# Performance work log

Hardware: AMD Instinct MI355X
Metric: run time of the kernel (lower is better)

Reference implementation:

```python
import jax, jax.numpy as jnp
import numpy as np

R = 6                 # max displacement / padding
D = 2 * R + 1         # window side; D*D = 169 displacements


def setup_inputs() -> dict:
    key = jax.random.key(0)
    k1, k2, k3 = jax.random.split(key, 3)
    b, cf, h, w = 2, 32, 256, 256
    feats_t = jax.random.normal(k1, (b, cf, h, w), jnp.float32)
    feats_r = jax.random.normal(k2, (b, cf, h, w), jnp.float32)
    img_r = jax.random.uniform(k3, (b, 1, h, w), jnp.float32)
    return {"feats_t": feats_t, "feats_r": feats_r, "img_r": img_r}


def _forward(feats_t, feats_r, img_r):
    b, cf, h, w = feats_t.shape
    ci = img_r.shape[1]
    x2p = jnp.pad(feats_r, ((0, 0), (0, 0), (R, R), (R, R)))
    imgp = jnp.pad(img_r, ((0, 0), (0, 0), (R, R), (R, R)))
    # displacement offsets in the same order as the torch double loop (_y outer, _x inner)
    offs = jnp.stack(
        jnp.meshgrid(jnp.arange(D), jnp.arange(D), indexing="ij"), axis=-1
    ).reshape(-1, 2)

    def step(carry, off):
        dy, dx = off[0], off[1]
        win = jax.lax.dynamic_slice(x2p, (0, 0, dy, dx), (b, cf, h, w))
        c = jnp.sum(feats_t * win, axis=1)  # [b, h, w] correlation for this displacement
        iw = jax.lax.dynamic_slice(imgp, (0, 0, dy, dx), (b, ci, h, w))
        return carry, (c, iw)

    _, (corr, imgs) = jax.lax.scan(step, 0, offs)  # corr: [D*D, b, h, w]; imgs: [D*D, b, ci, h, w]
    attn = jax.nn.softmax(corr, axis=0)  # softmax over displacements (torch dim=1 channel axis)
    # weighted sum of shifted reference images -> warped target image
    return jnp.einsum("dbhw,dbchw->bchw", attn, imgs)


def reference(feats_t, feats_r, img_r):
    return _forward(feats_t, feats_r, img_r)
```

## Files before the change

### kernel.cpp

```cpp
#include <hip/hip_runtime.h>
#include <stdint.h>

typedef _Float16 half_t;
typedef _Float16 v4h __attribute__((ext_vector_type(4)));
typedef float v4f __attribute__((ext_vector_type(4)));

#define HH 256
#define WW 256
#define HW (HH*WW)
#define CF 32
#define TH 16
#define TW 16
#define NROWS (TH+12)
#define NPX   (TW+16)
#define PXS   36
#define RSTEP (NPX*PXS)
#define NTHREADS 1024
#define L2E 1.44269504088896340736f

__global__ __launch_bounds__(NTHREADS, 8)
void corr_recon(const float* __restrict__ ft, const float* __restrict__ fr,
                const float* __restrict__ img, float* __restrict__ out)
{
    __shared__ half_t frl[NROWS * RSTEP];
    __shared__ float  img_lds[NROWS * NPX];

    const int bid0 = blockIdx.x;
    const int bid  = (bid0 & 7) * 64 + (bid0 >> 3);

    const int b0  = bid >> 8;
    const int rb  = bid & 255;
    const int y0  = (rb >> 4) * TH;
    const int x0t = (rb & 15) * TW;

    const int tid  = threadIdx.x;
    const int lane = tid & 63;
    const int w    = tid >> 6;
    const int n    = lane & 15;
    const int g    = lane >> 4;

    const float* frb = fr  + (size_t)b0 * CF * HW;
    const float* ftb = ft  + (size_t)b0 * CF * HW;
    const float* imb = img + (size_t)b0 * HW;

    for (int i = tid; i < NROWS * 8 * 8; i += NTHREADS) {
        const int px4 = i & 7;
        const int q   = (i >> 3) & 7;
        const int row = i >> 6;
        const int gy  = y0 - 6 + row;
        const int gx  = x0t - 6 + px4 * 4;
        const int gyc = min(max(gy, 0), HH-1);
        const bool oky = (gy == gyc);
        const float* src = frb + ((size_t)(4*q) * HH + gyc) * WW;
        float t[4][4];
        if (oky && gx >= 0 && gx + 3 < WW) {
            #pragma unroll
            for (int jc = 0; jc < 4; ++jc) {
                float4 v = *(const float4*)(src + (size_t)jc * HW + gx);
                t[jc][0]=v.x; t[jc][1]=v.y; t[jc][2]=v.z; t[jc][3]=v.w;
            }
        } else {
            #pragma unroll
            for (int jc = 0; jc < 4; ++jc)
                #pragma unroll
                for (int e = 0; e < 4; ++e) {
                    int x = gx + e;
                    t[jc][e] = (oky && x >= 0 && x < WW) ? src[(size_t)jc * HW + x] : 0.f;
                }
        }
        #pragma unroll
        for (int jp = 0; jp < 4; ++jp) {
            const int px = px4 * 4 + jp;
            v4h pk;
            pk[0] = (half_t)t[0][jp]; pk[1] = (half_t)t[1][jp];
            pk[2] = (half_t)t[2][jp]; pk[3] = (half_t)t[3][jp];
            *(v4h*)&frl[(row * NPX + px) * PXS + q * 4] = pk;
        }
    }
    for (int i = tid; i < NROWS * 8; i += NTHREADS) {
        const int px4 = i & 7;
        const int row = i >> 3;
        const int gy = y0 - 6 + row;
        const int gx = x0t - 6 + px4*4;
        const int gyc = min(max(gy, 0), HH-1);
        const bool oky = (gy == gyc);
        const float* p = imb + (size_t)gyc * WW;
        float v[4];
        if (oky && gx >= 0 && gx + 3 < WW) {
            float4 t4 = *(const float4*)(p + gx);
            v[0]=t4.x; v[1]=t4.y; v[2]=t4.z; v[3]=t4.w;
        } else {
            #pragma unroll
            for (int e = 0; e < 4; ++e) {
                int x = gx + e;
                v[e] = (oky && x >= 0 && x < WW) ? p[x] : 0.f;
            }
        }
        float4 f4; f4.x=v[0]; f4.y=v[1]; f4.z=v[2]; f4.w=v[3];
        *(float4*)&img_lds[row*NPX + px4*4] = f4;
    }

    const int y = y0 + w;
    v4h alo, ahi;
    {
        const float* fa = ftb + (size_t)y * WW + (x0t + n);
        #pragma unroll
        for (int j = 0; j < 4; ++j) {
            alo[j] = (half_t)(fa[(size_t)(4*g + j)      * HW] * L2E);
            ahi[j] = (half_t)(fa[(size_t)(16 + 4*g + j) * HW] * L2E);
        }
    }

    v4f bias0, bias1;
    #pragma unroll
    for (int r = 0; r < 4; ++r) {
        const int m  = 4*g + r;
        const int d0 = n - m;
        const int d1 = 16 + n - m;
        bias0[r] = (d0 >= 0 && d0 <= 12) ? 0.f : -1e4f;
        bias1[r] = (d1 >= 0 && d1 <= 12) ? 0.f : -1e4f;
    }
    const int dm = n - 4*g;

    __syncthreads();

    v4f lp = {0,0,0,0}, ap = {0,0,0,0};

    #pragma unroll 1
    for (int dy = 0; dy < 13; ++dy) {
        const half_t* pr = &frl[((w + dy) * NPX + n) * PXS + 4*g];
        v4h b0l = *(const v4h*)(pr);
        v4h b0h = *(const v4h*)(pr + 16);
        v4h b1l = *(const v4h*)(pr + 16*PXS);
        v4h b1h = *(const v4h*)(pr + 16*PXS + 16);

        v4f c0 = __builtin_amdgcn_mfma_f32_16x16x16f16(alo, b0l, bias0, 0, 0, 0);
        c0     = __builtin_amdgcn_mfma_f32_16x16x16f16(ahi, b0h, c0,    0, 0, 0);
        v4f c1 = __builtin_amdgcn_mfma_f32_16x16x16f16(alo, b1l, bias1, 0, 0, 0);
        c1     = __builtin_amdgcn_mfma_f32_16x16x16f16(ahi, b1h, c1,    0, 0, 0);

        const float* ir = &img_lds[(w + dy) * NPX + n];
        const float iw0 = ir[0];
        const float iw1 = ir[16];

        #pragma unroll
        for (int r = 0; r < 4; ++r) {
            const bool cond = (dm >= r);
            float cs  = cond ? c0[r] : c1[r];
            float iws = cond ? iw0   : iw1;
            float e = __builtin_amdgcn_exp2f(cs);
            lp[r] += e;
            ap[r] += e * iws;
        }
    }

    #pragma unroll
    for (int r = 0; r < 4; ++r) {
        float lv = lp[r], av = ap[r];
        lv += __shfl_xor(lv, 1);  av += __shfl_xor(av, 1);
        lv += __shfl_xor(lv, 2);  av += __shfl_xor(av, 2);
        lv += __shfl_xor(lv, 4);  av += __shfl_xor(av, 4);
        lv += __shfl_xor(lv, 8);  av += __shfl_xor(av, 8);
        lp[r] = lv; ap[r] = av;
    }
    if (n < 4) {
        const float lv = n==0 ? lp[0] : n==1 ? lp[1] : n==2 ? lp[2] : lp[3];
        const float av = n==0 ? ap[0] : n==1 ? ap[1] : n==2 ? ap[2] : ap[3];
        out[(size_t)b0 * HW + (size_t)y * WW + x0t + 4*g + n] = av / lv;
    }
}

extern "C" void kernel_launch(void* const* d_in, const int* in_sizes, int n_in,
                              void* d_out, int out_size, void* d_ws, size_t ws_size,
                              hipStream_t stream)
{
    const float* ft  = (const float*)d_in[0];
    const float* fr  = (const float*)d_in[1];
    const float* img = (const float*)d_in[2];
    float* out = (float*)d_out;
    (void)in_sizes; (void)n_in; (void)out_size; (void)d_ws; (void)ws_size;
    corr_recon<<<512, NTHREADS, 0, stream>>>(ft, fr, img, out);
}
```

Before: 19.67 us.

## Process two rows per wave with 16x16x32 MFMA and software-pipelined LDS loads

Doubles the tile height so each wave computes two output rows, reusing each loaded reference-feature row from LDS for both rows. Switches to the 16x16x32 f16 MFMA with a reordered, padded LDS channel layout so one 8-wide load feeds a single MFMA. Also prefetches the next row's operands ahead of use. The grid halves to 256 blocks, which lowers parallelism on a 256-CU part and raises per-block LDS and register use.

Measured after the change: 19.01 us. 3.4% less time.

```diff
diff --git a/kernel.cpp b/kernel.cpp
--- a/kernel.cpp
+++ b/kernel.cpp
@@ -3,33 +3,32 @@
 
 typedef _Float16 half_t;
 typedef _Float16 v4h __attribute__((ext_vector_type(4)));
+typedef _Float16 v8h __attribute__((ext_vector_type(8)));
 typedef float v4f __attribute__((ext_vector_type(4)));
 
 #define HH 256
 #define WW 256
 #define HW (HH*WW)
-#define CF 32
-#define TH 16
+#define TH 32
 #define TW 16
 #define NROWS (TH+12)
 #define NPX   (TW+16)
-#define PXS   36
-#define RSTEP (NPX*PXS)
+#define PXS   40
 #define NTHREADS 1024
 #define L2E 1.44269504088896340736f
 
-__global__ __launch_bounds__(NTHREADS, 8)
+__global__ __launch_bounds__(NTHREADS, 4)
 void corr_recon(const float* __restrict__ ft, const float* __restrict__ fr,
                 const float* __restrict__ img, float* __restrict__ out)
 {
-    __shared__ half_t frl[NROWS * RSTEP];
+    __shared__ half_t frl[NROWS * NPX * PXS];
     __shared__ float  img_lds[NROWS * NPX];
 
     const int bid0 = blockIdx.x;
-    const int bid  = (bid0 & 7) * 64 + (bid0 >> 3);
-
-    const int b0  = bid >> 8;
-    const int rb  = bid & 255;
+    const int bid  = (bid0 & 7) * 32 + (bid0 >> 3);
+
+    const int b0  = bid >> 7;
+    const int rb  = bid & 127;
     const int y0  = (rb >> 4) * TH;
     const int x0t = (rb & 15) * TW;
 
@@ -39,8 +38,8 @@
     const int n    = lane & 15;
     const int g    = lane >> 4;
 
-    const float* frb = fr  + (size_t)b0 * CF * HW;
-    const float* ftb = ft  + (size_t)b0 * CF * HW;
+    const float* frb = fr  + (size_t)b0 * 32 * HW;
+    const float* ftb = ft  + (size_t)b0 * 32 * HW;
     const float* imb = img + (size_t)b0 * HW;
 
     for (int i = tid; i < NROWS * 8 * 8; i += NTHREADS) {
@@ -68,13 +67,14 @@
                     t[jc][e] = (oky && x >= 0 && x < WW) ? src[(size_t)jc * HW + x] : 0.f;
                 }
         }
+        const int qo = 8*(q & 3) + 4*(q >> 2);
         #pragma unroll
         for (int jp = 0; jp < 4; ++jp) {
             const int px = px4 * 4 + jp;
             v4h pk;
             pk[0] = (half_t)t[0][jp]; pk[1] = (half_t)t[1][jp];
             pk[2] = (half_t)t[2][jp]; pk[3] = (half_t)t[3][jp];
-            *(v4h*)&frl[(row * NPX + px) * PXS + q * 4] = pk;
+            *(v4h*)&frl[(row * NPX + px) * PXS + qo] = pk;
         }
     }
     for (int i = tid; i < NROWS * 8; i += NTHREADS) {
@@ -100,14 +100,16 @@
         *(float4*)&img_lds[row*NPX + px4*4] = f4;
     }
 
-    const int y = y0 + w;
-    v4h alo, ahi;
+    const int y = y0 + 2*w;
+    v8h a0, a1;
     {
         const float* fa = ftb + (size_t)y * WW + (x0t + n);
         #pragma unroll
         for (int j = 0; j < 4; ++j) {
-            alo[j] = (half_t)(fa[(size_t)(4*g + j)      * HW] * L2E);
-            ahi[j] = (half_t)(fa[(size_t)(16 + 4*g + j) * HW] * L2E);
+            a0[j]   = (half_t)(fa[(size_t)(4*g + j)      * HW] * L2E);
+            a0[4+j] = (half_t)(fa[(size_t)(16 + 4*g + j) * HW] * L2E);
+            a1[j]   = (half_t)(fa[WW + (size_t)(4*g + j)      * HW] * L2E);
+            a1[4+j] = (half_t)(fa[WW + (size_t)(16 + 4*g + j) * HW] * L2E);
         }
     }
 
@@ -124,25 +126,13 @@
 
     __syncthreads();
 
-    v4f lp = {0,0,0,0}, ap = {0,0,0,0};
-
-    #pragma unroll 1
-    for (int dy = 0; dy < 13; ++dy) {
-        const half_t* pr = &frl[((w + dy) * NPX + n) * PXS + 4*g];
-        v4h b0l = *(const v4h*)(pr);
-        v4h b0h = *(const v4h*)(pr + 16);
-        v4h b1l = *(const v4h*)(pr + 16*PXS);
-        v4h b1h = *(const v4h*)(pr + 16*PXS + 16);
-
-        v4f c0 = __builtin_amdgcn_mfma_f32_16x16x16f16(alo, b0l, bias0, 0, 0, 0);
-        c0     = __builtin_amdgcn_mfma_f32_16x16x16f16(ahi, b0h, c0,    0, 0, 0);
-        v4f c1 = __builtin_amdgcn_mfma_f32_16x16x16f16(alo, b1l, bias1, 0, 0, 0);
-        c1     = __builtin_amdgcn_mfma_f32_16x16x16f16(ahi, b1h, c1,    0, 0, 0);
-
-        const float* ir = &img_lds[(w + dy) * NPX + n];
-        const float iw0 = ir[0];
-        const float iw1 = ir[16];
-
+    v4f lp0 = {0,0,0,0}, ap0 = {0,0,0,0};
+    v4f lp1 = {0,0,0,0}, ap1 = {0,0,0,0};
+
+    auto STEP = [&](const v8h& a, v4f& lp, v4f& ap,
+                    const v8h& B0, const v8h& B1, float iw0, float iw1) {
+        v4f c0 = __builtin_amdgcn_mfma_f32_16x16x32_f16(a, B0, bias0, 0, 0, 0);
+        v4f c1 = __builtin_amdgcn_mfma_f32_16x16x32_f16(a, B1, bias1, 0, 0, 0);
         #pragma unroll
         for (int r = 0; r < 4; ++r) {
             const bool cond = (dm >= r);
@@ -152,21 +142,55 @@
             lp[r] += e;
             ap[r] += e * iws;
         }
-    }
+    };
+
+    const half_t* prd = &frl[(2*w * NPX + n) * PXS + 8*g];
+    const float*  ird = &img_lds[2*w * NPX + n];
+
+    v8h C0 = *(const v8h*)(prd);
+    v8h C1 = *(const v8h*)(prd + 16*PXS);
+    float ci0 = ird[0], ci1 = ird[16];
+
+    prd += NPX*PXS; ird += NPX;
+    v8h N0 = *(const v8h*)(prd);
+    v8h N1 = *(const v8h*)(prd + 16*PXS);
+    float ni0 = ird[0], ni1 = ird[16];
+
+    STEP(a0, lp0, ap0, C0, C1, ci0, ci1);
+
+    #pragma unroll 1
+    for (int rr = 1; rr < 13; ++rr) {
+        C0 = N0; C1 = N1; ci0 = ni0; ci1 = ni1;
+        prd += NPX*PXS; ird += NPX;
+        N0 = *(const v8h*)(prd);
+        N1 = *(const v8h*)(prd + 16*PXS);
+        ni0 = ird[0]; ni1 = ird[16];
+        STEP(a0, lp0, ap0, C0, C1, ci0, ci1);
+        STEP(a1, lp1, ap1, C0, C1, ci0, ci1);
+    }
+    STEP(a1, lp1, ap1, N0, N1, ni0, ni1);
 
     #pragma unroll
     for (int r = 0; r < 4; ++r) {
-        float lv = lp[r], av = ap[r];
-        lv += __shfl_xor(lv, 1);  av += __shfl_xor(av, 1);
-        lv += __shfl_xor(lv, 2);  av += __shfl_xor(av, 2);
-        lv += __shfl_xor(lv, 4);  av += __shfl_xor(av, 4);
-        lv += __shfl_xor(lv, 8);  av += __shfl_xor(av, 8);
-        lp[r] = lv; ap[r] = av;
+        float l0 = lp0[r], v0 = ap0[r], l1 = lp1[r], v1 = ap1[r];
+        l0 += __shfl_xor(l0, 1);  v0 += __shfl_xor(v0, 1);
+        l1 += __shfl_xor(l1, 1);  v1 += __shfl_xor(v1, 1);
+        l0 += __shfl_xor(l0, 2);  v0 += __shfl_xor(v0, 2);
+        l1 += __shfl_xor(l1, 2);  v1 += __shfl_xor(v1, 2);
+        l0 += __shfl_xor(l0, 4);  v0 += __shfl_xor(v0, 4);
+        l1 += __shfl_xor(l1, 4);  v1 += __shfl_xor(v1, 4);
+        l0 += __shfl_xor(l0, 8);  v0 += __shfl_xor(v0, 8);
+        l1 += __shfl_xor(l1, 8);  v1 += __shfl_xor(v1, 8);
+        lp0[r] = l0; ap0[r] = v0; lp1[r] = l1; ap1[r] = v1;
     }
     if (n < 4) {
-        const float lv = n==0 ? lp[0] : n==1 ? lp[1] : n==2 ? lp[2] : lp[3];
-        const float av = n==0 ? ap[0] : n==1 ? ap[1] : n==2 ? ap[2] : ap[3];
-        out[(size_t)b0 * HW + (size_t)y * WW + x0t + 4*g + n] = av / lv;
+        const float l0 = n==0 ? lp0[0] : n==1 ? lp0[1] : n==2 ? lp0[2] : lp0[3];
+        const float v0 = n==0 ? ap0[0] : n==1 ? ap0[1] : n==2 ? ap0[2] : ap0[3];
+        const float l1 = n==0 ? lp1[0] : n==1 ? lp1[1] : n==2 ? lp1[2] : lp1[3];
+        const float v1 = n==0 ? ap1[0] : n==1 ? ap1[1] : n==2 ? ap1[2] : ap1[3];
+        float* orow = out + (size_t)b0 * HW + (size_t)y * WW + x0t + 4*g + n;
+        orow[0]  = v0 / l0;
+        orow[WW] = v1 / l1;
     }
 }
 
@@ -179,5 +203,5 @@
     const float* img = (const float*)d_in[2];
     float* out = (float*)d_out;
     (void)in_sizes; (void)n_in; (void)out_size; (void)d_ws; (void)ws_size;
-    corr_recon<<<512, NTHREADS, 0, stream>>>(ft, fr, img, out);
+    corr_recon<<<256, NTHREADS, 0, stream>>>(ft, fr, img, out);
 }
```
